# Kernel tuning notes

Hardware: AMD Instinct MI355X
Metric: run time of the kernel (lower is better)

## Reference

```python
import jax, jax.numpy as jnp
import numpy as np

B, S, H, NH = 8, 4096, 1024, 16
DH = H // NH  # head dim = 64
EPS = 1e-12


def setup_inputs() -> dict:
    key = jax.random.key(0)
    ks = jax.random.split(key, 10)
    sc = 1.0 / np.sqrt(H)
    return {
        "input_tensor": jax.random.normal(ks[0], (B, S, H), dtype=jnp.float32),
        "Wq": jax.random.normal(ks[1], (H, H), dtype=jnp.float32) * sc,
        "bq": jnp.zeros((H,), dtype=jnp.float32),
        "Wk": jax.random.normal(ks[2], (H, H), dtype=jnp.float32) * sc,
        "bk": jnp.zeros((H,), dtype=jnp.float32),
        "Wv": jax.random.normal(ks[3], (H, H), dtype=jnp.float32) * sc,
        "bv": jnp.zeros((H,), dtype=jnp.float32),
        "Wd": jax.random.normal(ks[4], (H, H), dtype=jnp.float32) * sc,
        "bd": jnp.zeros((H,), dtype=jnp.float32),
        "gamma": jnp.ones((H,), dtype=jnp.float32),
        "beta": jnp.zeros((H,), dtype=jnp.float32),
    }


def _heads(x):
    # [B,S,H] -> [B,NH,S,DH]
    return x.reshape(B, S, NH, DH).transpose(0, 2, 1, 3)


def reference(input_tensor, Wq, bq, Wk, bk, Wv, bv, Wd, bd, gamma, beta):
    q = _heads(input_tensor @ Wq + bq)  # [B,NH,S,DH]
    k = _heads(input_tensor @ Wk + bk)
    v = _heads(input_tensor @ Wv + bv)

    eq = jax.nn.elu(q)
    ek = jax.nn.elu(k)
    # L2-normalize per token along the head dim (matches norm over dim=3 of Q
    # and dim=2 of the [B,NH,DH,S]-permuted K in the torch code)
    qn = eq / jnp.linalg.norm(eq, axis=-1, keepdims=True)
    kn = ek / jnp.linalg.norm(ek, axis=-1, keepdims=True)

    kv = jnp.einsum("bhsd,bhse->bhde", kn, v)          # [B,NH,DH,DH]
    ctx = jnp.einsum("bhsd,bhde->bhse", qn, kv) / jnp.sqrt(jnp.float32(DH))
    ctx = ctx.transpose(0, 2, 1, 3).reshape(B, S, H)    # merge heads

    hidden = ctx @ Wd + bd
    x = hidden + input_tensor
    mu = jnp.mean(x, axis=-1, keepdims=True)
    var = jnp.mean(jnp.square(x - mu), axis=-1, keepdims=True)
    return (x - mu) / jnp.sqrt(var + EPS) * gamma + beta
```

## Files before the change

### kernel.cpp

```cpp
#include <hip/hip_runtime.h>
#include <cstdint>
#include <cstddef>

#define B_ 8
#define S_ 4096
#define H_ 1024
#define NH_ 16
#define DH_ 64
#define MTOK 32768

typedef unsigned short u16;
typedef __bf16 bf16x8 __attribute__((ext_vector_type(8)));
typedef u16 u16x8 __attribute__((ext_vector_type(8)));
typedef u16 u16x4 __attribute__((ext_vector_type(4)));
typedef float f32x4 __attribute__((ext_vector_type(4)));

#define DEVFN static __device__ __forceinline__

DEVFN float bf2f(u16 u) {
  union { uint32_t u; float f; } c; c.u = ((uint32_t)u) << 16; return c.f;
}
DEVFN u16 f2bf(float f) {
  union { float f; uint32_t u; } c; c.f = f;
  uint32_t r = c.u + 0x7fffu + ((c.u >> 16) & 1u);
  return (u16)(r >> 16);
}
DEVFN void gload16(const void* g, void* lds_p) {
  __builtin_amdgcn_global_load_lds(
      (const __attribute__((address_space(1))) void*)g,
      (__attribute__((address_space(3))) void*)lds_p, 16, 0, 0);
}

__global__ __launch_bounds__(256) void k_cvt_x(const float* __restrict__ x,
                                               u16* __restrict__ xb) {
  const size_t i = ((size_t)blockIdx.x * 256 + threadIdx.x) * 8;
  f32x4 a = *(const f32x4*)(x + i);
  f32x4 b = *(const f32x4*)(x + i + 4);
  u16x8 o;
#pragma unroll
  for (int j = 0; j < 4; ++j) { o[j] = f2bf(a[j]); o[4 + j] = f2bf(b[j]); }
  *(u16x8*)(xb + i) = o;
}

__global__ __launch_bounds__(256) void k_wt(const float* __restrict__ Wq,
                                            const float* __restrict__ Wk,
                                            const float* __restrict__ Wv,
                                            const float* __restrict__ Wd,
                                            u16* __restrict__ Wt,
                                            u16* __restrict__ Wdt) {
  const int n = blockIdx.x * 256 + threadIdx.x;
  const int kc = blockIdx.y;
  const int g = blockIdx.z;
  const float* W = (g == 0) ? Wq : (g == 1) ? Wk : (g == 2) ? Wv : Wd;
  u16x8 o;
#pragma unroll
  for (int j = 0; j < 8; ++j) o[j] = f2bf(W[(size_t)(kc * 8 + j) * 1024 + n]);
  u16* dst = (g < 3) ? (Wt + ((size_t)(g * 1024 + n)) * 1024 + kc * 8)
                     : (Wdt + (size_t)n * 1024 + kc * 8);
  *(u16x8*)dst = o;
}

template <int EPI>
__global__ __launch_bounds__(256, 2) void k_g(
    const u16* __restrict__ A, const u16* __restrict__ Bt,
    u16* __restrict__ o0, u16* __restrict__ o1, u16* __restrict__ o2,
    const float* __restrict__ b0, const float* __restrict__ b1,
    const float* __restrict__ b2) {
  __shared__ u16 As[128 * 32];
  __shared__ u16 Bs[128 * 32];
  const int tid = threadIdx.x;
  const int w = tid >> 6, l = tid & 63;
  const int wm = w >> 1, wn = w & 1;
  const long row0 = (long)blockIdx.x * 128;
  const long col0 = (long)blockIdx.y * 128;
  const u16* Bt2 = Bt + (EPI == 1 ? ((size_t)(row0 >> 12) << 20) : (size_t)0);

  f32x4 acc[4][4];
#pragma unroll
  for (int i = 0; i < 4; ++i)
#pragma unroll
    for (int j = 0; j < 4; ++j) acc[i][j] = (f32x4){0.f, 0.f, 0.f, 0.f};

  const int c0 = tid, c1 = 256 + tid;
  const u16* gA0 = A + (row0 + (c0 >> 2)) * 1024 + (c0 & 3) * 8;
  const u16* gA1 = A + (row0 + (c1 >> 2)) * 1024 + (c1 & 3) * 8;
  const u16* gB0 = Bt2 + (col0 + (c0 >> 2)) * 1024 + (c0 & 3) * 8;
  const u16* gB1 = Bt2 + (col0 + (c1 >> 2)) * 1024 + (c1 & 3) * 8;
  u16* lA0 = As + (w * 64) * 8;
  u16* lA1 = As + (256 + w * 64) * 8;
  u16* lB0 = Bs + (w * 64) * 8;
  u16* lB1 = Bs + (256 + w * 64) * 8;

  const int aoff = (wm * 64 + (l & 15)) * 32 + (l >> 4) * 8;
  const int boff = (wn * 64 + (l & 15)) * 32 + (l >> 4) * 8;

  for (int kt = 0; kt < 1024; kt += 32) {
    gload16(gA0 + kt, lA0);
    gload16(gA1 + kt, lA1);
    gload16(gB0 + kt, lB0);
    gload16(gB1 + kt, lB1);
    __syncthreads();
    bf16x8 af[4], bfr[4];
#pragma unroll
    for (int mi = 0; mi < 4; ++mi)
      af[mi] = *(const bf16x8*)(As + aoff + mi * 512);
#pragma unroll
    for (int ni = 0; ni < 4; ++ni)
      bfr[ni] = *(const bf16x8*)(Bs + boff + ni * 512);
#pragma unroll
    for (int mi = 0; mi < 4; ++mi)
#pragma unroll
      for (int ni = 0; ni < 4; ++ni)
        acc[mi][ni] = __builtin_amdgcn_mfma_f32_16x16x32_bf16(
            af[mi], bfr[ni], acc[mi][ni], 0, 0, 0);
    __syncthreads();
  }

  const int rb = (int)row0 + wm * 64 + ((l >> 4) << 2);
  const int cb = (int)col0 + wn * 64 + (l & 15);
  if (EPI == 0) {
    const int seg = (int)(col0 >> 10);
    const int cl = cb & 1023;
    u16* outp = (seg == 0) ? o0 : (seg == 1) ? o1 : o2;
    const float* bias = (seg == 0) ? b0 : (seg == 1) ? b1 : b2;
#pragma unroll
    for (int mi = 0; mi < 4; ++mi)
#pragma unroll
      for (int ni = 0; ni < 4; ++ni) {
        const float bv_ = bias[cl + ni * 16];
#pragma unroll
        for (int r = 0; r < 4; ++r) {
          float v = acc[mi][ni][r] + bv_;
          if (seg < 2) v = v > 0.f ? v : expm1f(v);
          outp[(size_t)(rb + mi * 16 + r) * 1024 + cl + ni * 16] = f2bf(v);
        }
      }
  } else {
#pragma unroll
    for (int mi = 0; mi < 4; ++mi)
#pragma unroll
      for (int ni = 0; ni < 4; ++ni)
#pragma unroll
        for (int r = 0; r < 4; ++r)
          o0[(size_t)(rb + mi * 16 + r) * 1024 + cb + ni * 16] =
              f2bf(acc[mi][ni][r]);
  }
}

__global__ __launch_bounds__(256) void k_qn(u16* __restrict__ eq) {
  const int tid = threadIdx.x, w = tid >> 6, l = tid & 63;
  const long t = (long)blockIdx.x * 4 + w;
  const size_t base = (size_t)t * 1024 + (l >> 2) * 64 + (l & 3) * 16;
  u16x8 a = *(const u16x8*)(eq + base);
  u16x8 b = *(const u16x8*)(eq + base + 8);
  float f[16];
#pragma unroll
  for (int j = 0; j < 8; ++j) { f[j] = bf2f(a[j]); f[8 + j] = bf2f(b[j]); }
  float ss = 0.f;
#pragma unroll
  for (int j = 0; j < 16; ++j) ss += f[j] * f[j];
  ss += __shfl_xor(ss, 1);
  ss += __shfl_xor(ss, 2);
  const float rq = rsqrtf(ss);
  u16x8 oa, ob;
#pragma unroll
  for (int j = 0; j < 8; ++j) { oa[j] = f2bf(f[j] * rq); ob[j] = f2bf(f[8 + j] * rq); }
  *(u16x8*)(eq + base) = oa;
  *(u16x8*)(eq + base + 8) = ob;
}

__global__ __launch_bounds__(256) void k_kv(const u16* __restrict__ ek,
                                            const u16* __restrict__ vv,
                                            float* __restrict__ kvp) {
  __shared__ __align__(16) char lds[69632];
  const int tid = threadIdx.x, w = tid >> 6, l = tid & 63;
  const int bid = blockIdx.x;
  const int sc = bid & 3, h = (bid >> 2) & 15, b = bid >> 6;
  const int tp = l >> 3, dgrp = l & 7;
  char* myk = lds + w * 17408;
  char* myv = myk + 8192;
  const long Tw = (long)b * 4096 + sc * 1024 + w * 256;
  const int d0 = dgrp * 8;

  f32x4 acc[4][4];
#pragma unroll
  for (int i = 0; i < 4; ++i)
#pragma unroll
    for (int j = 0; j < 4; ++j) acc[i][j] = (f32x4){0.f, 0.f, 0.f, 0.f};

  for (int st = 0; st < 4; ++st) {
#pragma unroll
    for (int ro = 0; ro < 4; ++ro) {
      const int tl = ro * 16 + tp * 2;
      const long T = Tw + st * 64 + tl;
      const u16* kp = ek + (size_t)T * 1024 + h * 64 + d0;
      const u16* vp = vv + (size_t)T * 1024 + h * 64 + d0;
      u16x8 k0 = *(const u16x8*)kp, k1 = *(const u16x8*)(kp + 1024);
      u16x8 v0 = *(const u16x8*)vp, v1 = *(const u16x8*)(vp + 1024);
      float f0[8], f1[8], s0 = 0.f, s1 = 0.f;
#pragma unroll
      for (int j = 0; j < 8; ++j) {
        f0[j] = bf2f(k0[j]); s0 += f0[j] * f0[j];
        f1[j] = bf2f(k1[j]); s1 += f1[j] * f1[j];
      }
      s0 += __shfl_xor(s0, 1); s0 += __shfl_xor(s0, 2); s0 += __shfl_xor(s0, 4);
      s1 += __shfl_xor(s1, 1); s1 += __shfl_xor(s1, 2); s1 += __shfl_xor(s1, 4);
      const float r0 = rsqrtf(s0), r1 = rsqrtf(s1);
#pragma unroll
      for (int j = 0; j < 8; ++j) {
        const int d = d0 + j;
        const int sw = (d & 8) ? 32 : 0;
        *(uint32_t*)(myk + d * 128 + ((tl * 2) ^ sw)) =
            (uint32_t)f2bf(f0[j] * r0) | ((uint32_t)f2bf(f1[j] * r1) << 16);
        *(uint32_t*)(myv + d * 128 + ((tl * 2) ^ sw)) =
            (uint32_t)v0[j] | ((uint32_t)v1[j] << 16);
      }
    }
#pragma unroll
    for (int ksl = 0; ksl < 2; ++ksl) {
      const int sb = (ksl * 64 + (l >> 4) * 16) ^ ((l & 8) ? 32 : 0);
      bf16x8 a[4], bb[4];
#pragma unroll
      for (int mf = 0; mf < 4; ++mf)
        a[mf] = *(const bf16x8*)(myk + (mf * 16 + (l & 15)) * 128 + sb);
#pragma unroll
      for (int nf = 0; nf < 4; ++nf)
        bb[nf] = *(const bf16x8*)(myv + (nf * 16 + (l & 15)) * 128 + sb);
#pragma unroll
      for (int mf = 0; mf < 4; ++mf)
#pragma unroll
        for (int nf = 0; nf < 4; ++nf)
          acc[mf][nf] = __builtin_amdgcn_mfma_f32_16x16x32_bf16(
              a[mf], bb[nf], acc[mf][nf], 0, 0, 0);
    }
  }

  __syncthreads();
  float* lf = (float*)(lds + w * 17408);
#pragma unroll
  for (int mf = 0; mf < 4; ++mf)
#pragma unroll
    for (int nf = 0; nf < 4; ++nf)
#pragma unroll
      for (int r = 0; r < 4; ++r)
        lf[(mf * 16 + (l >> 4) * 4 + r) * 68 + nf * 16 + (l & 15)] =
            acc[mf][nf][r];
  __syncthreads();
  float* op = kvp + ((size_t)(sc * 8 + b) * 16 + h) * 4096;
  const float* l0 = (const float*)lds;
  const int dd = tid >> 2, eb = (tid & 3) * 16;
#pragma unroll
  for (int c = 0; c < 4; ++c) {
    f32x4 s = *(const f32x4*)(l0 + dd * 68 + eb + c * 4);
#pragma unroll
    for (int w2 = 1; w2 < 4; ++w2)
      s += *(const f32x4*)(l0 + w2 * 4352 + dd * 68 + eb + c * 4);
    *(f32x4*)(op + tid * 16 + c * 4) = s;
  }
}

__global__ __launch_bounds__(256) void k_kvsum(const float* __restrict__ kvp,
                                               u16* __restrict__ kvb) {
  const size_t i = ((size_t)blockIdx.x * 256 + threadIdx.x) * 8;
  f32x4 s0 = *(const f32x4*)(kvp + i);
  f32x4 s1 = *(const f32x4*)(kvp + i + 4);
#pragma unroll
  for (int sc = 1; sc < 4; ++sc) {
    s0 += *(const f32x4*)(kvp + (size_t)sc * 524288 + i);
    s1 += *(const f32x4*)(kvp + (size_t)sc * 524288 + i + 4);
  }
  u16x8 o;
#pragma unroll
  for (int j = 0; j < 4; ++j) { o[j] = f2bf(s0[j]); o[4 + j] = f2bf(s1[j]); }
  *(u16x8*)(kvb + i) = o;
}

__global__ __launch_bounds__(256) void k_m2(const u16* __restrict__ kvb,
                                            const u16* __restrict__ Wdt,
                                            u16* __restrict__ M2t) {
  __shared__ __align__(16) u16 lds[12288];
  const int tid = threadIdx.x;
  const int w = tid >> 6, l = tid & 63;
  const int n0 = (int)blockIdx.x * 128, h = (int)blockIdx.y,
            b = (int)blockIdx.z;

  const u16* kvsrc = kvb + ((size_t)(b * 16 + h)) * 4096;
  gload16(kvsrc + (size_t)tid * 8, lds + (w * 64) * 8);
  gload16(kvsrc + (size_t)(256 + tid) * 8, lds + ((256 + w * 64)) * 8);
#pragma unroll
  for (int g = 0; g < 4; ++g) {
    const int c = g * 256 + tid;
    gload16(Wdt + (size_t)(n0 + (c >> 3)) * 1024 + h * 64 + (c & 7) * 8,
            lds + 4096 + (g * 256 + w * 64) * 8);
  }
  __syncthreads();

  f32x4 acc[4][2];
#pragma unroll
  for (int i = 0; i < 4; ++i)
#pragma unroll
    for (int j = 0; j < 2; ++j) acc[i][j] = (f32x4){0.f, 0.f, 0.f, 0.f};

#pragma unroll
  for (int kh = 0; kh < 2; ++kh) {
    bf16x8 a[4], bb[2];
#pragma unroll
    for (int mf = 0; mf < 4; ++mf)
      a[mf] = *(const bf16x8*)(lds + (mf * 16 + (l & 15)) * 64 + kh * 32 +
                               (l >> 4) * 8);
#pragma unroll
    for (int nf = 0; nf < 2; ++nf)
      bb[nf] = *(const bf16x8*)(lds + 4096 +
                                (w * 32 + nf * 16 + (l & 15)) * 64 + kh * 32 +
                                (l >> 4) * 8);
#pragma unroll
    for (int mf = 0; mf < 4; ++mf)
#pragma unroll
      for (int nf = 0; nf < 2; ++nf)
        acc[mf][nf] = __builtin_amdgcn_mfma_f32_16x16x32_bf16(
            a[mf], bb[nf], acc[mf][nf], 0, 0, 0);
  }

  u16* outb = M2t + ((size_t)b << 20) + h * 64;
#pragma unroll
  for (int mf = 0; mf < 4; ++mf)
#pragma unroll
    for (int nf = 0; nf < 2; ++nf) {
      const int col = w * 32 + nf * 16 + (l & 15);
      u16x4 o;
#pragma unroll
      for (int r = 0; r < 4; ++r) o[r] = f2bf(acc[mf][nf][r] * 0.125f);
      *(u16x4*)(outb + (size_t)(n0 + col) * 1024 + mf * 16 + (l >> 4) * 4) = o;
    }
}

__global__ __launch_bounds__(256) void k_ln(const u16* __restrict__ hid,
                                            const u16* __restrict__ xb,
                                            const float* __restrict__ bd,
                                            const float* __restrict__ g,
                                            const float* __restrict__ be,
                                            float* __restrict__ out) {
  const int tid = threadIdx.x, w = tid >> 6, l = tid & 63;
  const size_t base = (size_t)blockIdx.x * 1024 + tid * 4;
  u16x4 h4 = *(const u16x4*)(hid + base);
  u16x4 x4 = *(const u16x4*)(xb + base);
  f32x4 bd4 = *(const f32x4*)(bd + tid * 4);
  float v[4];
#pragma unroll
  for (int j = 0; j < 4; ++j) v[j] = bf2f(h4[j]) + bf2f(x4[j]) + bd4[j];
  float s = v[0] + v[1] + v[2] + v[3];
  float ss = v[0] * v[0] + v[1] * v[1] + v[2] * v[2] + v[3] * v[3];
#pragma unroll
  for (int o = 32; o > 0; o >>= 1) {
    s += __shfl_xor(s, o);
    ss += __shfl_xor(ss, o);
  }
  __shared__ float red[8];
  if (l == 0) { red[w] = s; red[w + 4] = ss; }
  __syncthreads();
  s = red[0] + red[1] + red[2] + red[3];
  ss = red[4] + red[5] + red[6] + red[7];
  const float mu = s * (1.0f / 1024.0f);
  const float var = ss * (1.0f / 1024.0f) - mu * mu;
  const float rstd = rsqrtf(var + 1e-12f);
  f32x4 g4 = *(const f32x4*)(g + tid * 4);
  f32x4 b4 = *(const f32x4*)(be + tid * 4);
  f32x4 o;
#pragma unroll
  for (int j = 0; j < 4; ++j) o[j] = (v[j] - mu) * rstd * g4[j] + b4[j];
  *(f32x4*)(out + base) = o;
}

extern "C" void kernel_launch(void* const* d_in, const int* in_sizes, int n_in,
                              void* d_out, int out_size, void* d_ws,
                              size_t ws_size, hipStream_t stream) {
  const float* X = (const float*)d_in[0];
  const float* Wq = (const float*)d_in[1];
  const float* bq = (const float*)d_in[2];
  const float* Wk = (const float*)d_in[3];
  const float* bk = (const float*)d_in[4];
  const float* Wv = (const float*)d_in[5];
  const float* bv = (const float*)d_in[6];
  const float* Wd = (const float*)d_in[7];
  const float* bd = (const float*)d_in[8];
  const float* gamma = (const float*)d_in[9];
  const float* beta = (const float*)d_in[10];
  float* out = (float*)d_out;

  char* ws = (char*)d_ws;
  u16* Xb = (u16*)(ws);
  u16* Wt = (u16*)(ws + 67108864);
  u16* eq = (u16*)(ws + 73400320);
  u16* ek = (u16*)(ws + 140509184);
  u16* kvb = (u16*)(ws + 206569472);
  u16* vb = (u16*)(ws + 207618048);
  u16* Wdt = (u16*)(ws + 274726912);
  float* kvp = (float*)(ws + 276824064);
  u16* M2t = (u16*)(ws + 285212672);

  k_cvt_x<<<16384, 256, 0, stream>>>(X, Xb);
  k_wt<<<dim3(4, 128, 4), 256, 0, stream>>>(Wq, Wk, Wv, Wd, Wt, Wdt);
  k_g<0><<<dim3(256, 24), 256, 0, stream>>>(Xb, Wt, eq, ek, vb, bq, bk, bv);
  k_qn<<<8192, 256, 0, stream>>>(eq);
  k_kv<<<512, 256, 0, stream>>>(ek, vb, kvp);
  k_kvsum<<<256, 256, 0, stream>>>(kvp, kvb);
  k_m2<<<dim3(8, 16, 8), 256, 0, stream>>>(kvb, Wdt, M2t);
  k_g<1><<<dim3(256, 8), 256, 0, stream>>>(eq, M2t, ek, nullptr, nullptr,
                                           nullptr, nullptr, nullptr);
  k_ln<<<32768, 256, 0, stream>>>(ek, Xb, bd, gamma, beta, out);
}
```

Baseline: 541.8 us.

## Deepen GEMM K-tile to 64 and fuse kv partial-sum into M2 kernel

The main GEMM kernel now stages a 64-deep K slice per iteration, two 32-wide halves, instead of 32. That halves the number of barrier pairs and loop iterations and issues more global loads per sync, at the cost of doubling LDS per block, which may affect 2-blocks-per-CU occupancy. Separately, the k_kvsum reduction kernel is removed. Its reduction of the four fp32 partial kv buffers and bf16 conversion now happens directly inside k_m2 into LDS, which drops one launch and the bf16 intermediate round-trip. Each M2 block redundantly re-reads the fp32 partials for its (b,h), eight times across blockIdx.x.

New measurement: 550.6 us. Within noise of the previous version (+1.6%).

```diff
diff --git a/kernel.cpp b/kernel.cpp
--- a/kernel.cpp
+++ b/kernel.cpp
@@ -66,8 +66,8 @@
     u16* __restrict__ o0, u16* __restrict__ o1, u16* __restrict__ o2,
     const float* __restrict__ b0, const float* __restrict__ b1,
     const float* __restrict__ b2) {
-  __shared__ u16 As[128 * 32];
-  __shared__ u16 Bs[128 * 32];
+  __shared__ u16 As[2 * 128 * 32];
+  __shared__ u16 Bs[2 * 128 * 32];
   const int tid = threadIdx.x;
   const int w = tid >> 6, l = tid & 63;
   const int wm = w >> 1, wn = w & 1;
@@ -81,38 +81,38 @@
 #pragma unroll
     for (int j = 0; j < 4; ++j) acc[i][j] = (f32x4){0.f, 0.f, 0.f, 0.f};
 
-  const int c0 = tid, c1 = 256 + tid;
-  const u16* gA0 = A + (row0 + (c0 >> 2)) * 1024 + (c0 & 3) * 8;
-  const u16* gA1 = A + (row0 + (c1 >> 2)) * 1024 + (c1 & 3) * 8;
-  const u16* gB0 = Bt2 + (col0 + (c0 >> 2)) * 1024 + (c0 & 3) * 8;
-  const u16* gB1 = Bt2 + (col0 + (c1 >> 2)) * 1024 + (c1 & 3) * 8;
-  u16* lA0 = As + (w * 64) * 8;
-  u16* lA1 = As + (256 + w * 64) * 8;
-  u16* lB0 = Bs + (w * 64) * 8;
-  u16* lB1 = Bs + (256 + w * 64) * 8;
+  const u16* gA = A + (row0 + (tid >> 2)) * 1024 + (tid & 3) * 8;
+  const u16* gB = Bt2 + (col0 + (tid >> 2)) * 1024 + (tid & 3) * 8;
+  u16* lA = As + w * 512;
+  u16* lB = Bs + w * 512;
 
   const int aoff = (wm * 64 + (l & 15)) * 32 + (l >> 4) * 8;
   const int boff = (wn * 64 + (l & 15)) * 32 + (l >> 4) * 8;
 
-  for (int kt = 0; kt < 1024; kt += 32) {
-    gload16(gA0 + kt, lA0);
-    gload16(gA1 + kt, lA1);
-    gload16(gB0 + kt, lB0);
-    gload16(gB1 + kt, lB1);
+  for (int kt = 0; kt < 1024; kt += 64) {
+#pragma unroll
+    for (int i = 0; i < 4; ++i) {
+      const int go = (i & 1) * 65536 + (i >> 1) * 32 + kt;
+      gload16(gA + go, lA + i * 2048);
+      gload16(gB + go, lB + i * 2048);
+    }
     __syncthreads();
-    bf16x8 af[4], bfr[4];
-#pragma unroll
-    for (int mi = 0; mi < 4; ++mi)
-      af[mi] = *(const bf16x8*)(As + aoff + mi * 512);
-#pragma unroll
-    for (int ni = 0; ni < 4; ++ni)
-      bfr[ni] = *(const bf16x8*)(Bs + boff + ni * 512);
-#pragma unroll
-    for (int mi = 0; mi < 4; ++mi)
+#pragma unroll
+    for (int kh = 0; kh < 2; ++kh) {
+      bf16x8 af[4], bfr[4];
+#pragma unroll
+      for (int mi = 0; mi < 4; ++mi)
+        af[mi] = *(const bf16x8*)(As + kh * 4096 + aoff + mi * 512);
 #pragma unroll
       for (int ni = 0; ni < 4; ++ni)
-        acc[mi][ni] = __builtin_amdgcn_mfma_f32_16x16x32_bf16(
-            af[mi], bfr[ni], acc[mi][ni], 0, 0, 0);
+        bfr[ni] = *(const bf16x8*)(Bs + kh * 4096 + boff + ni * 512);
+#pragma unroll
+      for (int mi = 0; mi < 4; ++mi)
+#pragma unroll
+        for (int ni = 0; ni < 4; ++ni)
+          acc[mi][ni] = __builtin_amdgcn_mfma_f32_16x16x32_bf16(
+              af[mi], bfr[ni], acc[mi][ni], 0, 0, 0);
+    }
     __syncthreads();
   }
 
@@ -259,23 +259,7 @@
   }
 }
 
-__global__ __launch_bounds__(256) void k_kvsum(const float* __restrict__ kvp,
-                                               u16* __restrict__ kvb) {
-  const size_t i = ((size_t)blockIdx.x * 256 + threadIdx.x) * 8;
-  f32x4 s0 = *(const f32x4*)(kvp + i);
-  f32x4 s1 = *(const f32x4*)(kvp + i + 4);
-#pragma unroll
-  for (int sc = 1; sc < 4; ++sc) {
-    s0 += *(const f32x4*)(kvp + (size_t)sc * 524288 + i);
-    s1 += *(const f32x4*)(kvp + (size_t)sc * 524288 + i + 4);
-  }
-  u16x8 o;
-#pragma unroll
-  for (int j = 0; j < 4; ++j) { o[j] = f2bf(s0[j]); o[4 + j] = f2bf(s1[j]); }
-  *(u16x8*)(kvb + i) = o;
-}
-
-__global__ __launch_bounds__(256) void k_m2(const u16* __restrict__ kvb,
+__global__ __launch_bounds__(256) void k_m2(const float* __restrict__ kvp,
                                             const u16* __restrict__ Wdt,
                                             u16* __restrict__ M2t) {
   __shared__ __align__(16) u16 lds[12288];
@@ -284,14 +268,28 @@
   const int n0 = (int)blockIdx.x * 128, h = (int)blockIdx.y,
             b = (int)blockIdx.z;
 
-  const u16* kvsrc = kvb + ((size_t)(b * 16 + h)) * 4096;
-  gload16(kvsrc + (size_t)tid * 8, lds + (w * 64) * 8);
-  gload16(kvsrc + (size_t)(256 + tid) * 8, lds + ((256 + w * 64)) * 8);
 #pragma unroll
   for (int g = 0; g < 4; ++g) {
     const int c = g * 256 + tid;
     gload16(Wdt + (size_t)(n0 + (c >> 3)) * 1024 + h * 64 + (c & 7) * 8,
             lds + 4096 + (g * 256 + w * 64) * 8);
+  }
+  const size_t kvbase = ((size_t)(b * 16 + h)) * 4096;
+#pragma unroll
+  for (int g = 0; g < 2; ++g) {
+    const int c = g * 256 + tid;
+    const float* p = kvp + kvbase + (size_t)(c >> 3) * 64 + (c & 7) * 8;
+    f32x4 s0 = *(const f32x4*)p;
+    f32x4 s1 = *(const f32x4*)(p + 4);
+#pragma unroll
+    for (int sc = 1; sc < 4; ++sc) {
+      s0 += *(const f32x4*)(p + (size_t)sc * 524288);
+      s1 += *(const f32x4*)(p + (size_t)sc * 524288 + 4);
+    }
+    u16x8 o;
+#pragma unroll
+    for (int j = 0; j < 4; ++j) { o[j] = f2bf(s0[j]); o[4 + j] = f2bf(s1[j]); }
+    *(u16x8*)(lds + c * 8) = o;
   }
   __syncthreads();
 
@@ -392,7 +390,6 @@
   u16* Wt = (u16*)(ws + 67108864);
   u16* eq = (u16*)(ws + 73400320);
   u16* ek = (u16*)(ws + 140509184);
-  u16* kvb = (u16*)(ws + 206569472);
   u16* vb = (u16*)(ws + 207618048);
   u16* Wdt = (u16*)(ws + 274726912);
   float* kvp = (float*)(ws + 276824064);
@@ -403,8 +400,7 @@
   k_g<0><<<dim3(256, 24), 256, 0, stream>>>(Xb, Wt, eq, ek, vb, bq, bk, bv);
   k_qn<<<8192, 256, 0, stream>>>(eq);
   k_kv<<<512, 256, 0, stream>>>(ek, vb, kvp);
-  k_kvsum<<<256, 256, 0, stream>>>(kvp, kvb);
-  k_m2<<<dim3(8, 16, 8), 256, 0, stream>>>(kvb, Wdt, M2t);
+  k_m2<<<dim3(8, 16, 8), 256, 0, stream>>>(kvp, Wdt, M2t);
   k_g<1><<<dim3(256, 8), 256, 0, stream>>>(eq, M2t, ek, nullptr, nullptr,
                                            nullptr, nullptr, nullptr);
   k_ln<<<32768, 256, 0, stream>>>(ek, Xb, bd, gamma, beta, out);
```
